# Kernel optimization log

Measured on AMD Instinct MI355X. Metric: run time of the kernel, lower is better.

Reference implementation:

```python
import jax, jax.numpy as jnp
import numpy as np

D, H, O, E, K = 512, 2048, 512, 8, 2
CF = 1.0  # capacity_factor


def setup_inputs() -> dict:
    key = jax.random.key(0)
    ks = jax.random.split(key, 4)
    s = lambda k, shape, sc: jax.random.normal(k, shape, jnp.float32) * sc
    return {
        "x": s(ks[0], (8, 2048, D), 1.0),
        "gate_w": s(ks[1], (D, E), D ** -0.5),
        "gate_b": jnp.zeros((E,), jnp.float32),
        "w1": s(ks[2], (E, D, H), D ** -0.5),
        "b1": jnp.zeros((E, H), jnp.float32),
        "w2": s(ks[3], (E, H, O), H ** -0.5),
        "b2": jnp.zeros((E, O), jnp.float32),
    }


def _moe(x, gate_w, gate_b, w1, b1, w2, b2):
    orig = x.shape
    xf = x.reshape(-1, orig[-1])            # [N, D]
    N = xf.shape[0]
    capacity = max(int((N / E) * CF), 4)    # static (shape-derived)

    logits = xf @ gate_w + gate_b           # [N, E]
    gate_probs = jax.nn.softmax(logits, axis=-1)
    topk_p, topk_i = jax.lax.top_k(gate_probs, K)          # [N, K]
    norm_p = topk_p / topk_p.sum(-1, keepdims=True)        # [N, K]

    hot = jax.nn.one_hot(topk_i, E, dtype=xf.dtype)        # [N, K, E]
    mask = hot.sum(1)                                      # [N, E] in {0,1} (top-k indices unique)
    w_te = (norm_p[..., None] * hot).sum(1)                # [N, E] routing weight per token/expert

    def dispatch(m):
        # m: [N] 0/1 mask for one expert; keep first `capacity` tokens in token order
        cs = jnp.cumsum(m)
        keep = (m > 0) & (cs <= capacity)
        idx = jnp.argsort(jnp.where(keep, 0, 1), stable=True)[:capacity]  # kept tokens first, in order
        valid = jnp.arange(capacity) < keep.sum()
        return idx, valid

    idx, valid = jax.vmap(dispatch)(mask.T)                # idx: [E, cap], valid: [E, cap]

    gathered = xf[idx]                                     # [E, cap, D]
    h = jax.nn.gelu(jnp.einsum('ecd,edh->ech', gathered, w1) + b1[:, None, :], approximate=False)
    out = jnp.einsum('ech,eho->eco', h, w2) + b2[:, None, :]  # [E, cap, O]

    wg = w_te[idx, jnp.arange(E)[:, None]]                 # [E, cap] gate weight per dispatched token
    contrib = out * (wg * valid.astype(out.dtype))[..., None]
    combined = jnp.zeros((N, O), out.dtype).at[idx.reshape(-1)].add(contrib.reshape(-1, O))
    return combined.reshape(*orig[:-1], O), gate_probs


def reference(x, gate_w, gate_b, w1, b1, w2, b2):
    return _moe(x, gate_w, gate_b, w1, b1, w2, b2)
```

## Files before the change

kernel.cpp:

```cpp
#include <hip/hip_runtime.h>
#include <hip/hip_bf16.h>

#define NTOK 16384
#define DDIM 512
#define HDIM 2048
#define ODIM 512
#define NE 8
#define CAP 2048

typedef __attribute__((ext_vector_type(8))) short short8v;
typedef __attribute__((ext_vector_type(4))) short short4v;
typedef __attribute__((ext_vector_type(8))) unsigned short ushort8v;
typedef __attribute__((ext_vector_type(4))) float f32x4;

static __device__ __forceinline__ unsigned short f2bf(float f) {
  __hip_bfloat16 h = __float2bfloat16(f);
  return __builtin_bit_cast(unsigned short, h);
}

#define GLOAD_LDS16(gp, lp)                                               \
  __builtin_amdgcn_global_load_lds(                                       \
      (const __attribute__((address_space(1))) void*)(gp),                \
      (__attribute__((address_space(3))) void*)(lp), 16, 0, 0)

__global__ void k_transpose_cvt(const float* __restrict__ src,
                                __hip_bfloat16* __restrict__ dst, int R, int C) {
  __shared__ float tile[32][33];
  int e = blockIdx.z;
  size_t base = (size_t)e * R * C;
  int c0 = blockIdx.x * 32, r0 = blockIdx.y * 32;
  int tx = threadIdx.x, ty = threadIdx.y;
#pragma unroll
  for (int i = 0; i < 32; i += 8)
    tile[ty + i][tx] = src[base + (size_t)(r0 + ty + i) * C + c0 + tx];
  __syncthreads();
#pragma unroll
  for (int i = 0; i < 32; i += 8)
    dst[base + (size_t)(c0 + ty + i) * R + r0 + tx] = __float2bfloat16(tile[tx][ty + i]);
}

__global__ void k_gate(const float* __restrict__ x, const float* __restrict__ gw,
                       const float* __restrict__ gb, float* __restrict__ gate_probs,
                       int2* __restrict__ tk_e, float2* __restrict__ tk_w,
                       int* __restrict__ token_slot) {
  __shared__ float gws[DDIM * 9];
  int tid = threadIdx.x;
  for (int i = tid; i < DDIM * NE; i += 256) {
    int d = i >> 3, e = i & 7;
    gws[d * 9 + e] = gw[i];
  }
  __syncthreads();
  int wid = tid >> 6, lane = tid & 63;
  int t = blockIdx.x * 4 + wid;
  const float* xr = x + (size_t)t * DDIM;
  float acc[NE] = {0.f, 0.f, 0.f, 0.f, 0.f, 0.f, 0.f, 0.f};
#pragma unroll
  for (int j = 0; j < 8; ++j) {
    float xv = xr[lane + 64 * j];
    const float* g = &gws[(lane + 64 * j) * 9];
#pragma unroll
    for (int e = 0; e < NE; ++e) acc[e] += xv * g[e];
  }
#pragma unroll
  for (int e = 0; e < NE; ++e) {
#pragma unroll
    for (int off = 32; off > 0; off >>= 1) acc[e] += __shfl_xor(acc[e], off, 64);
  }
  if (lane == 0) {
    float p[NE];
    float m = -1e30f;
#pragma unroll
    for (int e = 0; e < NE; ++e) { p[e] = acc[e] + gb[e]; m = fmaxf(m, p[e]); }
    float s = 0.f;
#pragma unroll
    for (int e = 0; e < NE; ++e) { p[e] = expf(p[e] - m); s += p[e]; }
    float inv = 1.f / s;
#pragma unroll
    for (int e = 0; e < NE; ++e) { p[e] *= inv; gate_probs[(size_t)t * NE + e] = p[e]; }
    int i1 = 0; float p1 = p[0];
#pragma unroll
    for (int e = 1; e < NE; ++e) if (p[e] > p1) { p1 = p[e]; i1 = e; }
    int i2 = -1; float p2 = -1e30f;
#pragma unroll
    for (int e = 0; e < NE; ++e) if (e != i1 && p[e] > p2) { p2 = p[e]; i2 = e; }
    float wsum = p1 + p2;
    tk_e[t] = make_int2(i1, i2);
    tk_w[t] = make_float2(p1 / wsum, p2 / wsum);
    token_slot[2 * t] = -1;
    token_slot[2 * t + 1] = -1;
  }
}

__global__ void k_dispatch(const int2* __restrict__ tk_e, int* __restrict__ token_slot,
                           int* __restrict__ expert_tokens) {
  int e = blockIdx.x;
  int tid = threadIdx.x;
  int lane = tid & 63, w = tid >> 6;
  __shared__ int wave_cnt[16];
  int base = 0;
  for (int chunk = 0; chunk < NTOK / 1024; ++chunk) {
    int t = chunk * 1024 + tid;
    int2 te = tk_e[t];
    int k = (te.x == e) ? 0 : ((te.y == e) ? 1 : -1);
    bool flag = (k >= 0);
    unsigned long long m = __ballot(flag);
    int pre = __popcll(m & ((1ull << lane) - 1ull));
    __syncthreads();
    if (lane == 0) wave_cnt[w] = __popcll(m);
    __syncthreads();
    int off = 0, total = 0;
#pragma unroll
    for (int i = 0; i < 16; ++i) {
      off += (i < w) ? wave_cnt[i] : 0;
      total += wave_cnt[i];
    }
    int rank = base + off + pre;
    if (flag && rank < CAP) {
      expert_tokens[e * CAP + rank] = t;
      token_slot[2 * t + k] = e * CAP + rank;
    }
    base += total;
  }
  int nvalid = base < CAP ? base : CAP;
  for (int s = nvalid + tid; s < CAP; s += 1024)
    expert_tokens[e * CAP + s] = 0;
}

__global__ void k_gather(const float* __restrict__ x,
                         const int* __restrict__ expert_tokens,
                         __hip_bfloat16* __restrict__ xg) {
  int tid = threadIdx.x, wid = tid >> 6, lane = tid & 63;
  int slot = blockIdx.x * 4 + wid;
  int tok = expert_tokens[slot];
  const float4* src = reinterpret_cast<const float4*>(x + (size_t)tok * DDIM) + lane * 2;
  float4 u = src[0], v = src[1];
  ushort8v o;
  o[0] = f2bf(u.x); o[1] = f2bf(u.y); o[2] = f2bf(u.z); o[3] = f2bf(u.w);
  o[4] = f2bf(v.x); o[5] = f2bf(v.y); o[6] = f2bf(v.z); o[7] = f2bf(v.w);
  *reinterpret_cast<ushort8v*>(xg + (size_t)slot * DDIM + lane * 8) = o;
}

static __device__ __forceinline__ float gelu_fast(float v) {
  float z = 1.5957691216057308f * (v + 0.044715f * v * v * v);
  return v / (1.f + __expf(-z));
}

template <int K, int M, bool GELU, typename OutT>
__global__ __launch_bounds__(256, 3) void k_gemm(
    const __hip_bfloat16* __restrict__ A, const __hip_bfloat16* __restrict__ B,
    const float* __restrict__ bias, OutT* __restrict__ C) {
  __shared__ char lds[3][16384];
  int gx = gridDim.x, gy = gridDim.y;
  int lin = (blockIdx.z * gy + blockIdx.y) * gx + blockIdx.x;
  int total = gx * gy * (int)gridDim.z;
  int cpx = total >> 3;
  lin = (lin & 7) * cpx + (lin >> 3);
  int gxy = gx * gy;
  int e = lin / gxy;
  int rem = lin - e * gxy;
  int mt = rem / gx, nt = rem - mt * gx;

  const int m0 = mt * 128, n0 = nt * 128;
  const int tid = threadIdx.x;
  const int lane = tid & 63, wid = tid >> 6;
  const int wr = wid >> 1, wc = wid & 1;
  const int lrow = lane & 15, kseg = lane >> 4;

  const int r0 = tid >> 2;
  const int sc = (tid & 3) ^ ((r0 >> 1) & 3);
  const int cb0 = (tid & 192) * 16;
  const int cb1 = 4096 + cb0;
  const __hip_bfloat16* Ab = A + ((size_t)e * M + m0) * K;
  const __hip_bfloat16* Bb = B + ((size_t)e * CAP + n0) * K;

#define STAGE(buf, kk)                                                         \
  do {                                                                         \
    GLOAD_LDS16(Ab + (size_t)r0 * K + (kk) + sc * 8, lds[buf] + cb0);          \
    GLOAD_LDS16(Ab + (size_t)(r0 + 64) * K + (kk) + sc * 8, lds[buf] + cb1);   \
    GLOAD_LDS16(Bb + (size_t)r0 * K + (kk) + sc * 8, lds[buf] + 8192 + cb0);   \
    GLOAD_LDS16(Bb + (size_t)(r0 + 64) * K + (kk) + sc * 8, lds[buf] + 8192 + cb1); \
  } while (0)

#define READF(fa, fb, bi)                                                      \
  do {                                                                         \
    const char* AsB_ = lds[bi];                                                \
    const char* BsB_ = lds[bi] + 8192;                                         \
    _Pragma("unroll")                                                          \
    for (int mm = 0; mm < 4; ++mm) {                                           \
      int rr = wr * 64 + mm * 16 + lrow;                                       \
      int ks = kseg ^ ((rr >> 1) & 3);                                         \
      fa[mm] = *reinterpret_cast<const short8v*>(AsB_ + rr * 64 + ks * 16);    \
    }                                                                          \
    _Pragma("unroll")                                                          \
    for (int nn = 0; nn < 4; ++nn) {                                           \
      int rr = wc * 64 + nn * 16 + lrow;                                       \
      int ks = kseg ^ ((rr >> 1) & 3);                                         \
      fb[nn] = *reinterpret_cast<const short8v*>(BsB_ + rr * 64 + ks * 16);    \
    }                                                                          \
  } while (0)

#define MFMA16(fa, fb)                                                         \
  do {                                                                         \
    __builtin_amdgcn_s_setprio(1);                                             \
    _Pragma("unroll")                                                          \
    for (int mm = 0; mm < 4; ++mm)                                             \
      _Pragma("unroll")                                                        \
      for (int nn = 0; nn < 4; ++nn)                                           \
        acc[mm][nn] = __builtin_amdgcn_mfma_f32_16x16x32_bf16(                 \
            fa[mm], fb[nn], acc[mm][nn], 0, 0, 0);                             \
    __builtin_amdgcn_s_setprio(0);                                             \
  } while (0)

#define LGKM0_FENCE()                                                          \
  do {                                                                         \
    asm volatile("s_waitcnt lgkmcnt(0)" ::: "memory");                         \
    __builtin_amdgcn_sched_barrier(0);                                         \
  } while (0)

  f32x4 acc[4][4] = {};
  short8v pa[4], pb[4], qa[4], qb[4];
  const int T = K >> 5;

  STAGE(0, 0);
  STAGE(1, 32);
  STAGE(2, 64);
  asm volatile("s_waitcnt vmcnt(8)" ::: "memory");
  __builtin_amdgcn_s_barrier();
  READF(pa, pb, 0);
  LGKM0_FENCE();

  int bt = 0;
  for (int t = 0; t < T; t += 2) {
    int b1 = (bt == 2) ? 0 : bt + 1;
    int b2 = (b1 == 2) ? 0 : b1 + 1;
    if (t + 2 < T) asm volatile("s_waitcnt vmcnt(4)" ::: "memory");
    else           asm volatile("s_waitcnt vmcnt(0)" ::: "memory");
    __builtin_amdgcn_s_barrier();
    READF(qa, qb, b1);
    if (t + 3 < T) STAGE(bt, (t + 3) * 32);
    __builtin_amdgcn_sched_barrier(0);
    MFMA16(pa, pb);
    LGKM0_FENCE();
    if (t + 2 < T) {
      if (t + 3 < T) asm volatile("s_waitcnt vmcnt(4)" ::: "memory");
      else           asm volatile("s_waitcnt vmcnt(0)" ::: "memory");
      __builtin_amdgcn_s_barrier();
      READF(pa, pb, b2);
      if (t + 4 < T) STAGE(b1, (t + 4) * 32);
      __builtin_amdgcn_sched_barrier(0);
    }
    MFMA16(qa, qb);
    LGKM0_FENCE();
    bt = b2;
  }
#undef STAGE
#undef READF
#undef MFMA16
#undef LGKM0_FENCE

#pragma unroll
  for (int mm = 0; mm < 4; ++mm) {
    int mrow = m0 + wr * 64 + mm * 16 + kseg * 4;
    float4 bv = *reinterpret_cast<const float4*>(&bias[e * M + mrow]);
#pragma unroll
    for (int nn = 0; nn < 4; ++nn) {
      int token = n0 + wc * 64 + nn * 16 + lrow;
      float v0 = acc[mm][nn][0] + bv.x;
      float v1 = acc[mm][nn][1] + bv.y;
      float v2 = acc[mm][nn][2] + bv.z;
      float v3 = acc[mm][nn][3] + bv.w;
      if (GELU) {
        v0 = gelu_fast(v0); v1 = gelu_fast(v1);
        v2 = gelu_fast(v2); v3 = gelu_fast(v3);
      }
      OutT* cp = C + ((size_t)e * CAP + token) * M + mrow;
      if constexpr (__is_same(OutT, __hip_bfloat16)) {
        short4v o;
        o[0] = (short)f2bf(v0); o[1] = (short)f2bf(v1);
        o[2] = (short)f2bf(v2); o[3] = (short)f2bf(v3);
        *reinterpret_cast<short4v*>(cp) = o;
      } else {
        float4 o = {v0, v1, v2, v3};
        *reinterpret_cast<float4*>(cp) = o;
      }
    }
  }
}

__global__ void k_combine(const float* __restrict__ outbuf,
                          const int* __restrict__ token_slot,
                          const float2* __restrict__ tk_w,
                          float* __restrict__ comb) {
  int tid = threadIdx.x;
  int wid = tid >> 6, lane = tid & 63;
  int t = blockIdx.x * 4 + wid;
  int s0 = token_slot[2 * t], s1 = token_slot[2 * t + 1];
  float2 w = tk_w[t];
  float r[8] = {0.f, 0.f, 0.f, 0.f, 0.f, 0.f, 0.f, 0.f};
  if (s0 >= 0) {
    const float4* p = reinterpret_cast<const float4*>(outbuf + (size_t)s0 * ODIM + lane * 8);
    float4 a = p[0], b = p[1];
    r[0] += w.x * a.x; r[1] += w.x * a.y; r[2] += w.x * a.z; r[3] += w.x * a.w;
    r[4] += w.x * b.x; r[5] += w.x * b.y; r[6] += w.x * b.z; r[7] += w.x * b.w;
  }
  if (s1 >= 0) {
    const float4* p = reinterpret_cast<const float4*>(outbuf + (size_t)s1 * ODIM + lane * 8);
    float4 a = p[0], b = p[1];
    r[0] += w.y * a.x; r[1] += w.y * a.y; r[2] += w.y * a.z; r[3] += w.y * a.w;
    r[4] += w.y * b.x; r[5] += w.y * b.y; r[6] += w.y * b.z; r[7] += w.y * b.w;
  }
  float4* q = reinterpret_cast<float4*>(comb + (size_t)t * ODIM + lane * 8);
  float4 o0 = {r[0], r[1], r[2], r[3]};
  float4 o1 = {r[4], r[5], r[6], r[7]};
  q[0] = o0;
  q[1] = o1;
}

extern "C" void kernel_launch(void* const* d_in, const int* in_sizes, int n_in,
                              void* d_out, int out_size, void* d_ws, size_t ws_size,
                              hipStream_t stream) {
  const float* x      = (const float*)d_in[0];
  const float* gate_w = (const float*)d_in[1];
  const float* gate_b = (const float*)d_in[2];
  const float* w1     = (const float*)d_in[3];
  const float* b1     = (const float*)d_in[4];
  const float* w2     = (const float*)d_in[5];
  const float* b2     = (const float*)d_in[6];

  float* comb = (float*)d_out;
  float* gate_probs = comb + (size_t)NTOK * ODIM;

  char* ws = (char*)d_ws;
  __hip_bfloat16* w1t    = (__hip_bfloat16*)(ws);
  __hip_bfloat16* w2t    = (__hip_bfloat16*)(ws + 16777216);
  __hip_bfloat16* hbuf   = (__hip_bfloat16*)(ws + 33554432);
  __hip_bfloat16* xg     = (__hip_bfloat16*)(ws + 100663296);
  float*          outbuf = (float*)(ws + 100663296);
  int*   expert_tokens   = (int*)(ws + 134217728);
  int2*  tk_e            = (int2*)(ws + 134283264);
  float2* tk_w           = (float2*)(ws + 134414336);
  int*   token_slot      = (int*)(ws + 134545408);

  k_transpose_cvt<<<dim3(HDIM / 32, DDIM / 32, NE), dim3(32, 8), 0, stream>>>(w1, w1t, DDIM, HDIM);
  k_transpose_cvt<<<dim3(ODIM / 32, HDIM / 32, NE), dim3(32, 8), 0, stream>>>(w2, w2t, HDIM, ODIM);
  k_gate<<<NTOK / 4, 256, 0, stream>>>(x, gate_w, gate_b, gate_probs, tk_e, tk_w, token_slot);
  k_dispatch<<<NE, 1024, 0, stream>>>(tk_e, token_slot, expert_tokens);
  k_gather<<<NE * CAP / 4, 256, 0, stream>>>(x, expert_tokens, xg);
  k_gemm<DDIM, HDIM, true, __hip_bfloat16>
      <<<dim3(CAP / 128, HDIM / 128, NE), 256, 0, stream>>>(w1t, xg, b1, hbuf);
  k_gemm<HDIM, ODIM, false, float>
      <<<dim3(CAP / 128, ODIM / 128, NE), 256, 0, stream>>>(w2t, hbuf, b2, outbuf);
  k_combine<<<NTOK / 4, 256, 0, stream>>>(outbuf, token_slot, tk_w, comb);
}
```

Baseline: 174.4 us.

## Fuse combine into second GEMM epilogue via atomics and merge prep kernels

```diff
diff --git a/kernel.cpp b/kernel.cpp
--- a/kernel.cpp
+++ b/kernel.cpp
@@ -23,13 +23,15 @@
       (const __attribute__((address_space(1))) void*)(gp),                \
       (__attribute__((address_space(3))) void*)(lp), 16, 0, 0)
 
-__global__ void k_transpose_cvt(const float* __restrict__ src,
-                                __hip_bfloat16* __restrict__ dst, int R, int C) {
+__device__ __forceinline__ void transpose_block(const float* __restrict__ src,
+                                                __hip_bfloat16* __restrict__ dst,
+                                                int R, int C, int b) {
   __shared__ float tile[32][33];
-  int e = blockIdx.z;
+  int nx = C >> 5, ny = R >> 5;
+  int x = b % nx, y = (b / nx) % ny, e = b / (nx * ny);
   size_t base = (size_t)e * R * C;
-  int c0 = blockIdx.x * 32, r0 = blockIdx.y * 32;
-  int tx = threadIdx.x, ty = threadIdx.y;
+  int c0 = x * 32, r0 = y * 32;
+  int tx = threadIdx.x & 31, ty = threadIdx.x >> 5;
 #pragma unroll
   for (int i = 0; i < 32; i += 8)
     tile[ty + i][tx] = src[base + (size_t)(r0 + ty + i) * C + c0 + tx];
@@ -39,10 +41,15 @@
     dst[base + (size_t)(c0 + ty + i) * R + r0 + tx] = __float2bfloat16(tile[tx][ty + i]);
 }
 
-__global__ void k_gate(const float* __restrict__ x, const float* __restrict__ gw,
-                       const float* __restrict__ gb, float* __restrict__ gate_probs,
-                       int2* __restrict__ tk_e, float2* __restrict__ tk_w,
-                       int* __restrict__ token_slot) {
+__global__ void k_prep(const float* __restrict__ x, const float* __restrict__ gw,
+                       const float* __restrict__ gb, const float* __restrict__ w1,
+                       __hip_bfloat16* __restrict__ w1t, const float* __restrict__ w2,
+                       __hip_bfloat16* __restrict__ w2t, float* __restrict__ gate_probs,
+                       int2* __restrict__ tk_e, float2* __restrict__ tk_w) {
+  int b = blockIdx.x;
+  if (b < 8192) { transpose_block(w1, w1t, DDIM, HDIM, b); return; }
+  if (b < 16384) { transpose_block(w2, w2t, HDIM, ODIM, b - 8192); return; }
+  b -= 16384;
   __shared__ float gws[DDIM * 9];
   int tid = threadIdx.x;
   for (int i = tid; i < DDIM * NE; i += 256) {
@@ -51,7 +58,7 @@
   }
   __syncthreads();
   int wid = tid >> 6, lane = tid & 63;
-  int t = blockIdx.x * 4 + wid;
+  int t = b * 4 + wid;
   const float* xr = x + (size_t)t * DDIM;
   float acc[NE] = {0.f, 0.f, 0.f, 0.f, 0.f, 0.f, 0.f, 0.f};
 #pragma unroll
@@ -86,13 +93,11 @@
     float wsum = p1 + p2;
     tk_e[t] = make_int2(i1, i2);
     tk_w[t] = make_float2(p1 / wsum, p2 / wsum);
-    token_slot[2 * t] = -1;
-    token_slot[2 * t + 1] = -1;
-  }
-}
-
-__global__ void k_dispatch(const int2* __restrict__ tk_e, int* __restrict__ token_slot,
-                           int* __restrict__ expert_tokens) {
+  }
+}
+
+__global__ void k_dispatch(const int2* __restrict__ tk_e, const float2* __restrict__ tk_w,
+                           int* __restrict__ expert_tokens, float* __restrict__ slot_w) {
   int e = blockIdx.x;
   int tid = threadIdx.x;
   int lane = tid & 63, w = tid >> 6;
@@ -101,6 +106,7 @@
   for (int chunk = 0; chunk < NTOK / 1024; ++chunk) {
     int t = chunk * 1024 + tid;
     int2 te = tk_e[t];
+    float2 wv = tk_w[t];
     int k = (te.x == e) ? 0 : ((te.y == e) ? 1 : -1);
     bool flag = (k >= 0);
     unsigned long long m = __ballot(flag);
@@ -117,13 +123,15 @@
     int rank = base + off + pre;
     if (flag && rank < CAP) {
       expert_tokens[e * CAP + rank] = t;
-      token_slot[2 * t + k] = e * CAP + rank;
+      slot_w[e * CAP + rank] = (k == 0) ? wv.x : wv.y;
     }
     base += total;
   }
   int nvalid = base < CAP ? base : CAP;
-  for (int s = nvalid + tid; s < CAP; s += 1024)
+  for (int s = nvalid + tid; s < CAP; s += 1024) {
     expert_tokens[e * CAP + s] = 0;
+    slot_w[e * CAP + s] = 0.f;
+  }
 }
 
 __global__ void k_gather(const float* __restrict__ x,
@@ -145,10 +153,12 @@
   return v / (1.f + __expf(-z));
 }
 
-template <int K, int M, bool GELU, typename OutT>
+template <int K, int M, bool GELU, bool FUSE, typename OutT>
 __global__ __launch_bounds__(256, 3) void k_gemm(
     const __hip_bfloat16* __restrict__ A, const __hip_bfloat16* __restrict__ B,
-    const float* __restrict__ bias, OutT* __restrict__ C) {
+    const float* __restrict__ bias, OutT* __restrict__ C,
+    const int* __restrict__ expert_tokens, const float* __restrict__ slot_w,
+    float* __restrict__ comb) {
   __shared__ char lds[3][16384];
   int gx = gridDim.x, gy = gridDim.y;
   int lin = (blockIdx.z * gy + blockIdx.y) * gx + blockIdx.x;
@@ -258,62 +268,56 @@
 #undef MFMA16
 #undef LGKM0_FENCE
 
-#pragma unroll
-  for (int mm = 0; mm < 4; ++mm) {
-    int mrow = m0 + wr * 64 + mm * 16 + kseg * 4;
-    float4 bv = *reinterpret_cast<const float4*>(&bias[e * M + mrow]);
+  if constexpr (FUSE) {
+    int tokslot[4]; float sw[4];
 #pragma unroll
     for (int nn = 0; nn < 4; ++nn) {
-      int token = n0 + wc * 64 + nn * 16 + lrow;
-      float v0 = acc[mm][nn][0] + bv.x;
-      float v1 = acc[mm][nn][1] + bv.y;
-      float v2 = acc[mm][nn][2] + bv.z;
-      float v3 = acc[mm][nn][3] + bv.w;
-      if (GELU) {
-        v0 = gelu_fast(v0); v1 = gelu_fast(v1);
-        v2 = gelu_fast(v2); v3 = gelu_fast(v3);
+      int ts = e * CAP + n0 + wc * 64 + nn * 16 + lrow;
+      tokslot[nn] = expert_tokens[ts];
+      sw[nn] = slot_w[ts];
+    }
+#pragma unroll
+    for (int mm = 0; mm < 4; ++mm) {
+      int mrow = m0 + wr * 64 + mm * 16 + kseg * 4;
+      float4 bv = *reinterpret_cast<const float4*>(&bias[e * M + mrow]);
+#pragma unroll
+      for (int nn = 0; nn < 4; ++nn) {
+        float* cp = comb + (size_t)tokslot[nn] * ODIM + mrow;
+        atomicAdd(cp + 0, (acc[mm][nn][0] + bv.x) * sw[nn]);
+        atomicAdd(cp + 1, (acc[mm][nn][1] + bv.y) * sw[nn]);
+        atomicAdd(cp + 2, (acc[mm][nn][2] + bv.z) * sw[nn]);
+        atomicAdd(cp + 3, (acc[mm][nn][3] + bv.w) * sw[nn]);
       }
-      OutT* cp = C + ((size_t)e * CAP + token) * M + mrow;
-      if constexpr (__is_same(OutT, __hip_bfloat16)) {
-        short4v o;
-        o[0] = (short)f2bf(v0); o[1] = (short)f2bf(v1);
-        o[2] = (short)f2bf(v2); o[3] = (short)f2bf(v3);
-        *reinterpret_cast<short4v*>(cp) = o;
-      } else {
-        float4 o = {v0, v1, v2, v3};
-        *reinterpret_cast<float4*>(cp) = o;
+    }
+  } else {
+#pragma unroll
+    for (int mm = 0; mm < 4; ++mm) {
+      int mrow = m0 + wr * 64 + mm * 16 + kseg * 4;
+      float4 bv = *reinterpret_cast<const float4*>(&bias[e * M + mrow]);
+#pragma unroll
+      for (int nn = 0; nn < 4; ++nn) {
+        int token = n0 + wc * 64 + nn * 16 + lrow;
+        float v0 = acc[mm][nn][0] + bv.x;
+        float v1 = acc[mm][nn][1] + bv.y;
+        float v2 = acc[mm][nn][2] + bv.z;
+        float v3 = acc[mm][nn][3] + bv.w;
+        if (GELU) {
+          v0 = gelu_fast(v0); v1 = gelu_fast(v1);
+          v2 = gelu_fast(v2); v3 = gelu_fast(v3);
+        }
+        OutT* cp = C + ((size_t)e * CAP + token) * M + mrow;
+        if constexpr (__is_same(OutT, __hip_bfloat16)) {
+          short4v o;
+          o[0] = (short)f2bf(v0); o[1] = (short)f2bf(v1);
+          o[2] = (short)f2bf(v2); o[3] = (short)f2bf(v3);
+          *reinterpret_cast<short4v*>(cp) = o;
+        } else {
+          float4 o = {v0, v1, v2, v3};
+          *reinterpret_cast<float4*>(cp) = o;
+        }
       }
     }
   }
-}
-
-__global__ void k_combine(const float* __restrict__ outbuf,
-                          const int* __restrict__ token_slot,
-                          const float2* __restrict__ tk_w,
-                          float* __restrict__ comb) {
-  int tid = threadIdx.x;
-  int wid = tid >> 6, lane = tid & 63;
-  int t = blockIdx.x * 4 + wid;
-  int s0 = token_slot[2 * t], s1 = token_slot[2 * t + 1];
-  float2 w = tk_w[t];
-  float r[8] = {0.f, 0.f, 0.f, 0.f, 0.f, 0.f, 0.f, 0.f};
-  if (s0 >= 0) {
-    const float4* p = reinterpret_cast<const float4*>(outbuf + (size_t)s0 * ODIM + lane * 8);
-    float4 a = p[0], b = p[1];
-    r[0] += w.x * a.x; r[1] += w.x * a.y; r[2] += w.x * a.z; r[3] += w.x * a.w;
-    r[4] += w.x * b.x; r[5] += w.x * b.y; r[6] += w.x * b.z; r[7] += w.x * b.w;
-  }
-  if (s1 >= 0) {
-    const float4* p = reinterpret_cast<const float4*>(outbuf + (size_t)s1 * ODIM + lane * 8);
-    float4 a = p[0], b = p[1];
-    r[0] += w.y * a.x; r[1] += w.y * a.y; r[2] += w.y * a.z; r[3] += w.y * a.w;
-    r[4] += w.y * b.x; r[5] += w.y * b.y; r[6] += w.y * b.z; r[7] += w.y * b.w;
-  }
-  float4* q = reinterpret_cast<float4*>(comb + (size_t)t * ODIM + lane * 8);
-  float4 o0 = {r[0], r[1], r[2], r[3]};
-  float4 o1 = {r[4], r[5], r[6], r[7]};
-  q[0] = o0;
-  q[1] = o1;
 }
 
 extern "C" void kernel_launch(void* const* d_in, const int* in_sizes, int n_in,
@@ -335,20 +339,21 @@
   __hip_bfloat16* w2t    = (__hip_bfloat16*)(ws + 16777216);
   __hip_bfloat16* hbuf   = (__hip_bfloat16*)(ws + 33554432);
   __hip_bfloat16* xg     = (__hip_bfloat16*)(ws + 100663296);
-  float*          outbuf = (float*)(ws + 100663296);
   int*   expert_tokens   = (int*)(ws + 134217728);
   int2*  tk_e            = (int2*)(ws + 134283264);
   float2* tk_w           = (float2*)(ws + 134414336);
-  int*   token_slot      = (int*)(ws + 134545408);
-
-  k_transpose_cvt<<<dim3(HDIM / 32, DDIM / 32, NE), dim3(32, 8), 0, stream>>>(w1, w1t, DDIM, HDIM);
-  k_transpose_cvt<<<dim3(ODIM / 32, HDIM / 32, NE), dim3(32, 8), 0, stream>>>(w2, w2t, HDIM, ODIM);
-  k_gate<<<NTOK / 4, 256, 0, stream>>>(x, gate_w, gate_b, gate_probs, tk_e, tk_w, token_slot);
-  k_dispatch<<<NE, 1024, 0, stream>>>(tk_e, token_slot, expert_tokens);
+  float* slot_w          = (float*)(ws + 134545408);
+
+  hipMemsetAsync(comb, 0, (size_t)NTOK * ODIM * sizeof(float), stream);
+
+  k_prep<<<16384 + NTOK / 4, 256, 0, stream>>>(x, gate_w, gate_b, w1, w1t, w2, w2t,
+                                               gate_probs, tk_e, tk_w);
+  k_dispatch<<<NE, 1024, 0, stream>>>(tk_e, tk_w, expert_tokens, slot_w);
   k_gather<<<NE * CAP / 4, 256, 0, stream>>>(x, expert_tokens, xg);
-  k_gemm<DDIM, HDIM, true, __hip_bfloat16>
-      <<<dim3(CAP / 128, HDIM / 128, NE), 256, 0, stream>>>(w1t, xg, b1, hbuf);
-  k_gemm<HDIM, ODIM, false, float>
-      <<<dim3(CAP / 128, ODIM / 128, NE), 256, 0, stream>>>(w2t, hbuf, b2, outbuf);
-  k_combine<<<NTOK / 4, 256, 0, stream>>>(outbuf, token_slot, tk_w, comb);
-}
+  k_gemm<DDIM, HDIM, true, false, __hip_bfloat16>
+      <<<dim3(CAP / 128, HDIM / 128, NE), 256, 0, stream>>>(
+          w1t, xg, b1, hbuf, nullptr, nullptr, nullptr);
+  k_gemm<HDIM, ODIM, false, true, float>
+      <<<dim3(CAP / 128, ODIM / 128, NE), 256, 0, stream>>>(
+          w2t, hbuf, b2, (float*)nullptr, expert_tokens, slot_w, comb);
+}
```

Result: slower. 254.5 us (+45.9%).

## Fuse weight transposes with gating into one launch; store expert outputs in bf16

Applied to the files above, without the earlier changes.

```diff
diff --git a/kernel.cpp b/kernel.cpp
--- a/kernel.cpp
+++ b/kernel.cpp
@@ -17,19 +17,25 @@
   __hip_bfloat16 h = __float2bfloat16(f);
   return __builtin_bit_cast(unsigned short, h);
 }
+static __device__ __forceinline__ float bf2f(unsigned short u) {
+  unsigned int x = ((unsigned int)u) << 16;
+  return __builtin_bit_cast(float, x);
+}
 
 #define GLOAD_LDS16(gp, lp)                                               \
   __builtin_amdgcn_global_load_lds(                                       \
       (const __attribute__((address_space(1))) void*)(gp),                \
       (__attribute__((address_space(3))) void*)(lp), 16, 0, 0)
 
-__global__ void k_transpose_cvt(const float* __restrict__ src,
-                                __hip_bfloat16* __restrict__ dst, int R, int C) {
+__device__ __forceinline__ void transpose_block(const float* __restrict__ src,
+                                                __hip_bfloat16* __restrict__ dst,
+                                                int R, int C, int b) {
   __shared__ float tile[32][33];
-  int e = blockIdx.z;
+  int nx = C >> 5, ny = R >> 5;
+  int x = b % nx, y = (b / nx) % ny, e = b / (nx * ny);
   size_t base = (size_t)e * R * C;
-  int c0 = blockIdx.x * 32, r0 = blockIdx.y * 32;
-  int tx = threadIdx.x, ty = threadIdx.y;
+  int c0 = x * 32, r0 = y * 32;
+  int tx = threadIdx.x & 31, ty = threadIdx.x >> 5;
 #pragma unroll
   for (int i = 0; i < 32; i += 8)
     tile[ty + i][tx] = src[base + (size_t)(r0 + ty + i) * C + c0 + tx];
@@ -39,10 +45,16 @@
     dst[base + (size_t)(c0 + ty + i) * R + r0 + tx] = __float2bfloat16(tile[tx][ty + i]);
 }
 
-__global__ void k_gate(const float* __restrict__ x, const float* __restrict__ gw,
-                       const float* __restrict__ gb, float* __restrict__ gate_probs,
+__global__ void k_prep(const float* __restrict__ x, const float* __restrict__ gw,
+                       const float* __restrict__ gb, const float* __restrict__ w1,
+                       __hip_bfloat16* __restrict__ w1t, const float* __restrict__ w2,
+                       __hip_bfloat16* __restrict__ w2t, float* __restrict__ gate_probs,
                        int2* __restrict__ tk_e, float2* __restrict__ tk_w,
                        int* __restrict__ token_slot) {
+  int b = blockIdx.x;
+  if (b < 8192) { transpose_block(w1, w1t, DDIM, HDIM, b); return; }
+  if (b < 16384) { transpose_block(w2, w2t, HDIM, ODIM, b - 8192); return; }
+  b -= 16384;
   __shared__ float gws[DDIM * 9];
   int tid = threadIdx.x;
   for (int i = tid; i < DDIM * NE; i += 256) {
@@ -51,7 +63,7 @@
   }
   __syncthreads();
   int wid = tid >> 6, lane = tid & 63;
-  int t = blockIdx.x * 4 + wid;
+  int t = b * 4 + wid;
   const float* xr = x + (size_t)t * DDIM;
   float acc[NE] = {0.f, 0.f, 0.f, 0.f, 0.f, 0.f, 0.f, 0.f};
 #pragma unroll
@@ -287,7 +299,7 @@
   }
 }
 
-__global__ void k_combine(const float* __restrict__ outbuf,
+__global__ void k_combine(const __hip_bfloat16* __restrict__ outbuf,
                           const int* __restrict__ token_slot,
                           const float2* __restrict__ tk_w,
                           float* __restrict__ comb) {
@@ -298,16 +310,14 @@
   float2 w = tk_w[t];
   float r[8] = {0.f, 0.f, 0.f, 0.f, 0.f, 0.f, 0.f, 0.f};
   if (s0 >= 0) {
-    const float4* p = reinterpret_cast<const float4*>(outbuf + (size_t)s0 * ODIM + lane * 8);
-    float4 a = p[0], b = p[1];
-    r[0] += w.x * a.x; r[1] += w.x * a.y; r[2] += w.x * a.z; r[3] += w.x * a.w;
-    r[4] += w.x * b.x; r[5] += w.x * b.y; r[6] += w.x * b.z; r[7] += w.x * b.w;
+    ushort8v a = *reinterpret_cast<const ushort8v*>(outbuf + (size_t)s0 * ODIM + lane * 8);
+#pragma unroll
+    for (int j = 0; j < 8; ++j) r[j] += w.x * bf2f(a[j]);
   }
   if (s1 >= 0) {
-    const float4* p = reinterpret_cast<const float4*>(outbuf + (size_t)s1 * ODIM + lane * 8);
-    float4 a = p[0], b = p[1];
-    r[0] += w.y * a.x; r[1] += w.y * a.y; r[2] += w.y * a.z; r[3] += w.y * a.w;
-    r[4] += w.y * b.x; r[5] += w.y * b.y; r[6] += w.y * b.z; r[7] += w.y * b.w;
+    ushort8v a = *reinterpret_cast<const ushort8v*>(outbuf + (size_t)s1 * ODIM + lane * 8);
+#pragma unroll
+    for (int j = 0; j < 8; ++j) r[j] += w.y * bf2f(a[j]);
   }
   float4* q = reinterpret_cast<float4*>(comb + (size_t)t * ODIM + lane * 8);
   float4 o0 = {r[0], r[1], r[2], r[3]};
@@ -335,20 +345,19 @@
   __hip_bfloat16* w2t    = (__hip_bfloat16*)(ws + 16777216);
   __hip_bfloat16* hbuf   = (__hip_bfloat16*)(ws + 33554432);
   __hip_bfloat16* xg     = (__hip_bfloat16*)(ws + 100663296);
-  float*          outbuf = (float*)(ws + 100663296);
+  __hip_bfloat16* outbuf = (__hip_bfloat16*)(ws + 117440512);
   int*   expert_tokens   = (int*)(ws + 134217728);
   int2*  tk_e            = (int2*)(ws + 134283264);
   float2* tk_w           = (float2*)(ws + 134414336);
   int*   token_slot      = (int*)(ws + 134545408);
 
-  k_transpose_cvt<<<dim3(HDIM / 32, DDIM / 32, NE), dim3(32, 8), 0, stream>>>(w1, w1t, DDIM, HDIM);
-  k_transpose_cvt<<<dim3(ODIM / 32, HDIM / 32, NE), dim3(32, 8), 0, stream>>>(w2, w2t, HDIM, ODIM);
-  k_gate<<<NTOK / 4, 256, 0, stream>>>(x, gate_w, gate_b, gate_probs, tk_e, tk_w, token_slot);
+  k_prep<<<16384 + NTOK / 4, 256, 0, stream>>>(x, gate_w, gate_b, w1, w1t, w2, w2t,
+                                               gate_probs, tk_e, tk_w, token_slot);
   k_dispatch<<<NE, 1024, 0, stream>>>(tk_e, token_slot, expert_tokens);
   k_gather<<<NE * CAP / 4, 256, 0, stream>>>(x, expert_tokens, xg);
   k_gemm<DDIM, HDIM, true, __hip_bfloat16>
       <<<dim3(CAP / 128, HDIM / 128, NE), 256, 0, stream>>>(w1t, xg, b1, hbuf);
-  k_gemm<HDIM, ODIM, false, float>
+  k_gemm<HDIM, ODIM, false, __hip_bfloat16>
       <<<dim3(CAP / 128, ODIM / 128, NE), 256, 0, stream>>>(w2t, hbuf, b2, outbuf);
   k_combine<<<NTOK / 4, 256, 0, stream>>>(outbuf, token_slot, tk_w, comb);
 }
```

After: 167.8 us. 1.04x faster.
